# Optimization experiments

Hardware: AMD Instinct MI355X
Metric: run time of the kernel (lower is better)

The kernel has to match this reference:

```python
import jax, jax.numpy as jnp
import numpy as np
import math

B, S, HID, NH = 2, 2048, 1024, 16
HD = HID // NH  # head_dim = 64
TEMPERATURE = 1.0


def setup_inputs() -> dict:
    key = jax.random.key(0)
    ks = jax.random.split(key, 6)
    w = lambda k: (jax.random.normal(k, (HID, HID), dtype=jnp.float32) * 0.02)
    return {
        "hidden_states": jax.random.normal(ks[0], (B, S, HID), dtype=jnp.float32),
        "attention_mask": jnp.ones((B, S), dtype=jnp.float32),
        "Wq": w(ks[1]), "bq": jnp.zeros((HID,), jnp.float32),
        "Wk": w(ks[2]), "bk": jnp.zeros((HID,), jnp.float32),
        "Wv": w(ks[3]), "bv": jnp.zeros((HID,), jnp.float32),
        "Wo": w(ks[4]), "bo": jnp.zeros((HID,), jnp.float32),
    }


def reference(hidden_states, attention_mask, Wq, bq, Wk, bk, Wv, bv, Wo, bo):
    b, s, hid = hidden_states.shape
    heads = lambda x: x.reshape(b, s, NH, HD).transpose(0, 2, 1, 3)  # [b,h,s,d]

    q = heads(hidden_states @ Wq.T + bq)
    k = heads(hidden_states @ Wk.T + bk)
    v = heads(hidden_states @ Wv.T + bv)

    # padding mask applied multiplicatively to k and v
    m = attention_mask[:, None, :, None]  # [b,1,s,1]
    k = k * m
    v = v * m

    # auxiliary Hopfield state: k^T @ v per head -> [b,h,d,d]
    state = jnp.einsum("bhsd,bhse->bhde", k, v)

    # energy / scores
    energy = jnp.einsum("bhqd,bhkd->bhqk", q, k) / (TEMPERATURE * math.sqrt(HD))
    causal = jnp.triu(jnp.ones((s, s), dtype=bool), k=1)  # True above diagonal
    energy = jnp.where(causal[None, None], -jnp.inf, energy)
    energy = jnp.where(attention_mask[:, None, None, :] == 0, -jnp.inf, energy)

    attn = jax.nn.softmax(energy, axis=-1)
    out = jnp.einsum("bhqk,bhkd->bhqd", attn, v)
    out = out.transpose(0, 2, 1, 3).reshape(b, s, hid)
    out = out @ Wo.T + bo
    return out, state
```

## Files before the change

### kernel.cpp

```cpp
#include <hip/hip_runtime.h>
#include <hip/hip_bf16.h>

#define B_ 2
#define S_ 2048
#define HID_ 1024
#define NH_ 16
#define HD_ 64
#define MTOK (B_*S_)
#define LDQKV 3072

typedef __attribute__((ext_vector_type(8))) __bf16 bf16x8;
typedef __attribute__((ext_vector_type(4))) __bf16 bf16x4;
typedef __attribute__((ext_vector_type(4))) float f32x4;

__device__ __forceinline__ void gl16(__bf16* lds, const __bf16* g) {
  __builtin_amdgcn_global_load_lds(
      (const __attribute__((address_space(1))) void*)g,
      (__attribute__((address_space(3))) void*)lds, 16, 0, 0);
}

__global__ __launch_bounds__(256) void cast_all(
    const float* __restrict__ X,
    const float* __restrict__ Wq, const float* __restrict__ Wk,
    const float* __restrict__ Wv, const float* __restrict__ Wo,
    __bf16* __restrict__ Xb, __bf16* __restrict__ Wqkvb, __bf16* __restrict__ Wob)
{
  int i = blockIdx.x * 256 + threadIdx.x;
  const float* src; __bf16* dst; int j;
  if (i < (1 << 20))              { src = X;  dst = Xb;                 j = i; }
  else if (i < (1<<20)+(1<<18))   { src = Wq; dst = Wqkvb;              j = i - (1<<20); }
  else if (i < (1<<20)+(2<<18))   { src = Wk; dst = Wqkvb + (1<<20);    j = i - (1<<20) - (1<<18); }
  else if (i < (1<<20)+(3<<18))   { src = Wv; dst = Wqkvb + (2<<20);    j = i - (1<<20) - (2<<18); }
  else                            { src = Wo; dst = Wob;                j = i - (1<<20) - (3<<18); }
  float4 v = reinterpret_cast<const float4*>(src)[j];
  bf16x4 o;
  o[0] = (__bf16)v.x; o[1] = (__bf16)v.y; o[2] = (__bf16)v.z; o[3] = (__bf16)v.w;
  reinterpret_cast<bf16x4*>(dst)[j] = o;
}

__global__ __launch_bounds__(256) void gemm_qkv(
    const __bf16* __restrict__ A, const __bf16* __restrict__ W,
    const float* __restrict__ bq, const float* __restrict__ bk,
    const float* __restrict__ bv, const float* __restrict__ mask,
    __bf16* __restrict__ C)
{
  __shared__ __bf16 As[2][128 * 32];
  __shared__ __bf16 Bs[2][128 * 32];
  const int t = threadIdx.x;
  const int m0 = blockIdx.y * 128;
  const int n0 = blockIdx.x * 128;
  const int lane = t & 63;
  const int w = t >> 6;
  const int wr = (w >> 1) * 64;
  const int wc = (w & 1) * 64;
  const int fr = lane & 15;
  const int kg = lane >> 4;

  f32x4 acc[4][4];
  #pragma unroll
  for (int i = 0; i < 4; i++)
    #pragma unroll
    for (int j = 0; j < 4; j++) acc[i][j] = (f32x4)0.f;

  const int srow = w * 16 + (lane >> 2);
  const int scol = (lane & 3) * 8;
  const __bf16* ap0 = A + (size_t)(m0 + srow) * HID_ + scol;
  const __bf16* ap1 = A + (size_t)(m0 + 64 + srow) * HID_ + scol;
  const __bf16* wp0 = W + (size_t)(n0 + srow) * HID_ + scol;
  const __bf16* wp1 = W + (size_t)(n0 + 64 + srow) * HID_ + scol;

  #define GSTAGE(buf, koff) \
    gl16(&As[buf][w * 512], ap0 + (koff)); \
    gl16(&As[buf][2048 + w * 512], ap1 + (koff)); \
    gl16(&Bs[buf][w * 512], wp0 + (koff)); \
    gl16(&Bs[buf][2048 + w * 512], wp1 + (koff));

  GSTAGE(0, 0);
  for (int k0 = 0; k0 < HID_; k0 += 32) {
    const int cur = (k0 >> 5) & 1;
    if (k0 + 32 < HID_) {
      GSTAGE(cur ^ 1, k0 + 32);
      asm volatile("s_waitcnt vmcnt(4)" ::: "memory");
    } else {
      asm volatile("s_waitcnt vmcnt(0)" ::: "memory");
    }
    __builtin_amdgcn_sched_barrier(0);
    __builtin_amdgcn_s_barrier();
    bf16x8 af[4], bf[4];
    #pragma unroll
    for (int m = 0; m < 4; m++) af[m] = *(const bf16x8*)&As[cur][(wr + m*16 + fr) * 32 + kg*8];
    #pragma unroll
    for (int n = 0; n < 4; n++) bf[n] = *(const bf16x8*)&Bs[cur][(wc + n*16 + fr) * 32 + kg*8];
    #pragma unroll
    for (int m = 0; m < 4; m++)
      #pragma unroll
      for (int n = 0; n < 4; n++)
        acc[m][n] = __builtin_amdgcn_mfma_f32_16x16x32_bf16(af[m], bf[n], acc[m][n], 0, 0, 0);
    __builtin_amdgcn_s_barrier();
  }

  const int region = n0 >> 10;
  const float* bias = region == 0 ? bq : (region == 1 ? bk : bv);
  const int nloc = n0 & 1023;

  #pragma unroll
  for (int m = 0; m < 4; m++) {
    #pragma unroll
    for (int r = 0; r < 4; r++) {
      int row = m0 + wr + m*16 + kg*4 + r;
      float rs = region ? mask[row] : 1.f;
      #pragma unroll
      for (int n = 0; n < 4; n++) {
        int c = wc + n*16 + fr;
        float v = (acc[m][n][r] + bias[nloc + c]) * rs;
        C[(size_t)row * LDQKV + n0 + c] = (__bf16)v;
      }
    }
  }
}

__global__ __launch_bounds__(256) void gemm_o(
    const __bf16* __restrict__ A, const __bf16* __restrict__ W,
    const float* __restrict__ bias, float* __restrict__ C)
{
  __shared__ __bf16 As[2][128 * 32];
  __shared__ __bf16 Bs[2][128 * 32];
  const int t = threadIdx.x;
  const int m0 = blockIdx.y * 128;
  const int n0 = blockIdx.x * 128;
  const int lane = t & 63;
  const int w = t >> 6;
  const int wr = (w >> 1) * 64;
  const int wc = (w & 1) * 64;
  const int fr = lane & 15;
  const int kg = lane >> 4;

  f32x4 acc[4][4];
  #pragma unroll
  for (int i = 0; i < 4; i++)
    #pragma unroll
    for (int j = 0; j < 4; j++) acc[i][j] = (f32x4)0.f;

  const int srow = w * 16 + (lane >> 2);
  const int scol = (lane & 3) * 8;
  const __bf16* ap0 = A + (size_t)(m0 + srow) * HID_ + scol;
  const __bf16* ap1 = A + (size_t)(m0 + 64 + srow) * HID_ + scol;
  const __bf16* wp0 = W + (size_t)(n0 + srow) * HID_ + scol;
  const __bf16* wp1 = W + (size_t)(n0 + 64 + srow) * HID_ + scol;

  GSTAGE(0, 0);
  for (int k0 = 0; k0 < HID_; k0 += 32) {
    const int cur = (k0 >> 5) & 1;
    if (k0 + 32 < HID_) {
      GSTAGE(cur ^ 1, k0 + 32);
      asm volatile("s_waitcnt vmcnt(4)" ::: "memory");
    } else {
      asm volatile("s_waitcnt vmcnt(0)" ::: "memory");
    }
    __builtin_amdgcn_sched_barrier(0);
    __builtin_amdgcn_s_barrier();
    bf16x8 af[4], bf[4];
    #pragma unroll
    for (int m = 0; m < 4; m++) af[m] = *(const bf16x8*)&As[cur][(wr + m*16 + fr) * 32 + kg*8];
    #pragma unroll
    for (int n = 0; n < 4; n++) bf[n] = *(const bf16x8*)&Bs[cur][(wc + n*16 + fr) * 32 + kg*8];
    #pragma unroll
    for (int m = 0; m < 4; m++)
      #pragma unroll
      for (int n = 0; n < 4; n++)
        acc[m][n] = __builtin_amdgcn_mfma_f32_16x16x32_bf16(af[m], bf[n], acc[m][n], 0, 0, 0);
    __builtin_amdgcn_s_barrier();
  }

  #pragma unroll
  for (int m = 0; m < 4; m++) {
    #pragma unroll
    for (int r = 0; r < 4; r++) {
      int row = m0 + wr + m*16 + kg*4 + r;
      #pragma unroll
      for (int n = 0; n < 4; n++) {
        int col = n0 + wc + n*16 + fr;
        C[(size_t)row * HID_ + col] = acc[m][n][r] + bias[col];
      }
    }
  }
}

__global__ __launch_bounds__(256) void transpose_kv(
    const __bf16* __restrict__ Kin, const __bf16* __restrict__ Vin,
    __bf16* __restrict__ Kt, __bf16* __restrict__ Vt)
{
  __shared__ __bf16 tile[64][68];
  const int tok0 = blockIdx.x * 64;
  const int f0 = blockIdx.y * 64;
  const __bf16* in = blockIdx.z ? Vin : Kin;
  __bf16* out = blockIdx.z ? Vt : Kt;
  const int t = threadIdx.x;
  const int r = t >> 2;
  const int c0 = (t & 3) * 16;
  const __bf16* src = in + (size_t)(tok0 + r) * LDQKV + f0 + c0;
  *(bf16x8*)&tile[r][c0]     = *(const bf16x8*)src;
  *(bf16x8*)&tile[r][c0 + 8] = *(const bf16x8*)(src + 8);
  __syncthreads();
  bf16x8 o0, o1;
  #pragma unroll
  for (int j = 0; j < 8; j++) { o0[j] = tile[c0 + j][r]; o1[j] = tile[c0 + 8 + j][r]; }
  __bf16* dst = out + (size_t)(f0 + r) * MTOK + tok0 + c0;
  *(bf16x8*)dst = o0;
  *(bf16x8*)(dst + 8) = o1;
}

#define SCALE_LOG2E 0.18033688011112043f

__device__ __forceinline__ bf16x8 ld_swz(const __bf16* base, int row, int xb) {
  return *(const bf16x8*)((const char*)base + row * 128 + (xb ^ ((row & 7) << 4)));
}
__device__ __forceinline__ void st_swz16(__bf16* base, int row, int colbyte, __bf16 v) {
  *(__bf16*)((char*)base + row * 128 + (colbyte ^ ((row & 7) << 4))) = v;
}
__device__ __forceinline__ bf16x8 ld_swz256(const __bf16* base, int row, int xb) {
  return *(const bf16x8*)((const char*)base + row * 256 + (xb ^ ((row & 7) << 4)));
}

__device__ __forceinline__ void attn_tile(
    const __bf16* __restrict__ ks, const __bf16* __restrict__ vs,
    const bool (&okm)[4], __bf16* __restrict__ pw,
    const bf16x8 (&qa)[2], f32x4 (&acc)[4], f32x4& accl,
    const bf16x8 ones, int q0w, int kt, int fc, int kg)
{
  f32x4 s[4];
  #pragma unroll
  for (int n = 0; n < 4; n++) s[n] = (f32x4)0.f;
  #pragma unroll
  for (int kd = 0; kd < 2; kd++)
    #pragma unroll
    for (int n = 0; n < 4; n++) {
      bf16x8 kf = ld_swz(ks, n * 16 + fc, kd * 64 + kg * 16);
      s[n] = __builtin_amdgcn_mfma_f32_16x16x32_bf16(qa[kd], kf, s[n], 0, 0, 0);
    }

  const int g4 = kg * 4;
  const bool fullt = (kt * 64 + 63 <= q0w);
  if (fullt) {
    #pragma unroll
    for (int r = 0; r < 4; r++)
      #pragma unroll
      for (int n = 0; n < 4; n++) {
        float p = okm[n] ? __builtin_amdgcn_exp2f(s[n][r] * SCALE_LOG2E) : 0.f;
        st_swz16(pw, g4 + r, (n * 16 + fc) * 2, (__bf16)p);
      }
  } else {
    #pragma unroll
    for (int r = 0; r < 4; r++) {
      const int qg = q0w + g4 + r;
      #pragma unroll
      for (int n = 0; n < 4; n++) {
        bool ok = okm[n] && (kt * 64 + n * 16 + fc <= qg);
        float p = ok ? __builtin_amdgcn_exp2f(s[n][r] * SCALE_LOG2E) : 0.f;
        st_swz16(pw, g4 + r, (n * 16 + fc) * 2, (__bf16)p);
      }
    }
  }

  #pragma unroll
  for (int kc = 0; kc < 2; kc++) {
    bf16x8 pf = ld_swz(pw, fc, kc * 64 + kg * 16);
    accl = __builtin_amdgcn_mfma_f32_16x16x32_bf16(pf, ones, accl, 0, 0, 0);
    #pragma unroll
    for (int n = 0; n < 4; n++) {
      bf16x8 vf = ld_swz(vs, n * 16 + fc, kc * 64 + kg * 16);
      acc[n] = __builtin_amdgcn_mfma_f32_16x16x32_bf16(pf, vf, acc[n], 0, 0, 0);
    }
  }
}

__global__ __launch_bounds__(256) void flash_mfma(
    const __bf16* __restrict__ Q, const __bf16* __restrict__ K,
    const __bf16* __restrict__ Vt, const float* __restrict__ mask,
    __bf16* __restrict__ O)
{
  __shared__ __bf16 Ks[2][64 * 64];
  __shared__ __bf16 Vs[2][64 * 64];
  __shared__ __bf16 Ps[4][16 * 64];

  const int bh = blockIdx.x;
  const int qt = 31 - (int)blockIdx.y;
  const int b = bh >> 4, h = bh & 15;
  const int t = threadIdx.x;
  const int w = t >> 6;
  const int lane = t & 63;
  const int fc = lane & 15;
  const int kg = lane >> 4;
  const int g4 = kg * 4;

  const int q0w = qt * 64 + w * 16;
  const size_t tokbase = (size_t)b * S_;

  const int rr = lane >> 3;
  const int cswz = ((lane & 7) ^ rr) * 8;
  const int ktmax = qt;

  bf16x8 qa[2];
  {
    const __bf16* qp = Q + (tokbase + q0w + fc) * LDQKV + h * HD_;
    qa[0] = *(const bf16x8*)(qp + kg * 8);
    qa[1] = *(const bf16x8*)(qp + 32 + kg * 8);
  }

  const float* mp = mask + tokbase + fc;
  float mnxt[4];
  #pragma unroll
  for (int n = 0; n < 4; n++) mnxt[n] = mp[n * 16];

  const __bf16* kp0 = K + (tokbase + (size_t)(w * 16 + rr)) * LDQKV + h * HD_ + cswz;
  const __bf16* kp1 = kp0 + (size_t)8 * LDQKV;
  const __bf16* vp0 = Vt + (size_t)(h * HD_ + w * 16 + rr) * MTOK + tokbase + cswz;
  const __bf16* vp1 = vp0 + (size_t)8 * MTOK;

  gl16(&Ks[0][(w * 16) * 64],     kp0);
  gl16(&Ks[0][(w * 16 + 8) * 64], kp1);
  gl16(&Vs[0][(w * 16) * 64],     vp0);
  gl16(&Vs[0][(w * 16 + 8) * 64], vp1);
  kp0 += (size_t)64 * LDQKV; kp1 += (size_t)64 * LDQKV;
  vp0 += 64; vp1 += 64;

  bf16x8 ones;
  #pragma unroll
  for (int j = 0; j < 8; j++) ones[j] = (__bf16)1.f;

  f32x4 acc[4], accl;
  #pragma unroll
  for (int n = 0; n < 4; n++) acc[n] = (f32x4)0.f;
  accl = (f32x4)0.f;

  __bf16* pw = &Ps[w][0];

  for (int kt = 0; kt <= ktmax; ++kt) {
    const int cur = kt & 1;
    float mcur[4];
    #pragma unroll
    for (int n = 0; n < 4; n++) mcur[n] = mnxt[n];

    if (kt < ktmax) {
      #pragma unroll
      for (int n = 0; n < 4; n++) mnxt[n] = mp[(kt + 1) * 64 + n * 16];
      const int nxt = cur ^ 1;
      gl16(&Ks[nxt][(w * 16) * 64],     kp0);
      gl16(&Ks[nxt][(w * 16 + 8) * 64], kp1);
      gl16(&Vs[nxt][(w * 16) * 64],     vp0);
      gl16(&Vs[nxt][(w * 16 + 8) * 64], vp1);
      kp0 += (size_t)64 * LDQKV; kp1 += (size_t)64 * LDQKV;
      vp0 += 64; vp1 += 64;
      asm volatile("s_waitcnt vmcnt(8)" ::: "memory");
    } else {
      asm volatile("s_waitcnt vmcnt(0)" ::: "memory");
    }
    __builtin_amdgcn_sched_barrier(0);
    __builtin_amdgcn_s_barrier();

    bool okm[4];
    #pragma unroll
    for (int n = 0; n < 4; n++) okm[n] = (mcur[n] != 0.f);

    attn_tile(&Ks[cur][0], &Vs[cur][0], okm, pw, qa, acc, accl, ones, q0w, kt, fc, kg);

    __builtin_amdgcn_s_barrier();
  }

  #pragma unroll
  for (int r = 0; r < 4; r++) {
    float inv = accl[r] > 0.f ? 1.f / accl[r] : 0.f;
    __bf16* op = O + (tokbase + q0w + g4 + r) * HID_ + h * HD_;
    #pragma unroll
    for (int n = 0; n < 4; n++)
      op[n * 16 + fc] = (__bf16)(acc[n][r] * inv);
  }
}

__global__ __launch_bounds__(256) void state_mfma(
    const __bf16* __restrict__ Kt, const __bf16* __restrict__ Vt,
    float* __restrict__ part)
{
  __shared__ __bf16 Kl[64 * 128];
  __shared__ __bf16 Vl[64 * 128];
  const int bh = blockIdx.x, sc = blockIdx.y;
  const int b = bh >> 4, h = bh & 15;
  const int t = threadIdx.x;
  const int w = t >> 6;
  const int lane = t & 63;
  const int fc = lane & 15;
  const int kg = lane >> 4;
  const size_t colbase = (size_t)b * S_ + sc * 128;
  const int rloc = lane >> 4;
  const int cb = (lane & 15) * 16;

  #pragma unroll
  for (int c = 0; c < 4; c++) {
    int row = w * 16 + c * 4 + rloc;
    int scol = (cb ^ ((row & 7) << 4)) >> 1;
    gl16(&Kl[(w * 16 + c * 4) * 128], Kt + (size_t)(h * HD_ + row) * MTOK + colbase + scol);
    gl16(&Vl[(w * 16 + c * 4) * 128], Vt + (size_t)(h * HD_ + row) * MTOK + colbase + scol);
  }
  __syncthreads();

  f32x4 acc[4];
  #pragma unroll
  for (int n = 0; n < 4; n++) acc[n] = (f32x4)0.f;
  #pragma unroll
  for (int ks = 0; ks < 4; ks++) {
    bf16x8 af = ld_swz256(Kl, w * 16 + fc, ks * 64 + kg * 16);
    #pragma unroll
    for (int n = 0; n < 4; n++) {
      bf16x8 bfr = ld_swz256(Vl, n * 16 + fc, ks * 64 + kg * 16);
      acc[n] = __builtin_amdgcn_mfma_f32_16x16x32_bf16(af, bfr, acc[n], 0, 0, 0);
    }
  }

  float* dst = part + (((size_t)bh * 16 + sc) << 12);
  #pragma unroll
  for (int n = 0; n < 4; n++)
    #pragma unroll
    for (int r = 0; r < 4; r++)
      dst[(w * 16 + kg * 4 + r) * 64 + n * 16 + fc] = acc[n][r];
}

__global__ __launch_bounds__(256) void state_reduce(
    const float* __restrict__ part, float* __restrict__ out)
{
  int i = blockIdx.x * 256 + threadIdx.x;
  int bh = i >> 12, de = i & 4095;
  float s = 0.f;
  #pragma unroll
  for (int sc = 0; sc < 16; sc++) s += part[(((size_t)bh * 16 + sc) << 12) + de];
  out[i] = s;
}

extern "C" void kernel_launch(void* const* d_in, const int* in_sizes, int n_in,
                              void* d_out, int out_size, void* d_ws, size_t ws_size,
                              hipStream_t stream)
{
  const float* hs   = (const float*)d_in[0];
  const float* mask = (const float*)d_in[1];
  const float* Wq   = (const float*)d_in[2];
  const float* bq   = (const float*)d_in[3];
  const float* Wk   = (const float*)d_in[4];
  const float* bk   = (const float*)d_in[5];
  const float* Wv   = (const float*)d_in[6];
  const float* bv   = (const float*)d_in[7];
  const float* Wo   = (const float*)d_in[8];
  const float* bo   = (const float*)d_in[9];
  float* out = (float*)d_out;

  char* ws = (char*)d_ws;
  __bf16* Wqkvb = (__bf16*)(ws);
  __bf16* Wob   = (__bf16*)(ws + (6u  << 20));
  __bf16* Xb    = (__bf16*)(ws + (8u  << 20));
  __bf16* QKV   = (__bf16*)(ws + (16u << 20));
  __bf16* Ob    = (__bf16*)(ws + (40u << 20));
  __bf16* Ktg   = (__bf16*)(ws + (48u << 20));

  cast_all<<<8192, 256, 0, stream>>>(hs, Wq, Wk, Wv, Wo, Xb, Wqkvb, Wob);

  gemm_qkv<<<dim3(LDQKV / 128, MTOK / 128), 256, 0, stream>>>(
      Xb, Wqkvb, bq, bk, bv, mask, QKV);

  __bf16* Vtg = Xb;
  transpose_kv<<<dim3(MTOK / 64, HID_ / 64, 2), 256, 0, stream>>>(
      QKV + 1024, QKV + 2048, Ktg, Vtg);

  flash_mfma<<<dim3(B_ * NH_, 32), 256, 0, stream>>>(
      QKV, QKV + 1024, Vtg, mask, Ob);

  gemm_o<<<dim3(HID_ / 128, MTOK / 128), 256, 0, stream>>>(Ob, Wob, bo, out);

  float* part = (float*)Ob;
  state_mfma<<<dim3(B_ * NH_, 16), 256, 0, stream>>>(Ktg, Vtg, part);
  state_reduce<<<512, 256, 0, stream>>>(part, out + (size_t)MTOK * HID_);
}
```

Before: 136.0 us.

## Fuse K transpose into QKV GEMM and state reduction into output GEMM

The QKV GEMM epilogue now writes K transposed through a swizzled LDS tile, so the separate transpose only handles V. The state partial reduction is folded into extra blocks of the output projection GEMM. state_mfma processes two chunks per block, halving the partials to reduce. s_setprio is raised around the MFMA sections in the flash attention kernel. Together these cut kernel launches and intermediate traffic, at the cost of a longer epilogue on the K-region GEMM blocks and some load imbalance.

```diff
diff --git a/kernel.cpp b/kernel.cpp
--- a/kernel.cpp
+++ b/kernel.cpp
@@ -38,12 +38,166 @@
   reinterpret_cast<bf16x4*>(dst)[j] = o;
 }
 
+__device__ __forceinline__ void st_T(__bf16* T, int row, int col, __bf16 v) {
+  *(__bf16*)((char*)T + row * 256 + ((col * 2) ^ (((row >> 3) & 15) << 4))) = v;
+}
+__device__ __forceinline__ __bf16 ld_T(const __bf16* T, int row, int col) {
+  return *(const __bf16*)((const char*)T + row * 256 + ((col * 2) ^ (((row >> 3) & 15) << 4)));
+}
+
 __global__ __launch_bounds__(256) void gemm_qkv(
     const __bf16* __restrict__ A, const __bf16* __restrict__ W,
     const float* __restrict__ bq, const float* __restrict__ bk,
     const float* __restrict__ bv, const float* __restrict__ mask,
-    __bf16* __restrict__ C)
-{
+    __bf16* __restrict__ C, __bf16* __restrict__ Kt)
+{
+  __shared__ __bf16 SMEM[16384];
+  __bf16* As0 = SMEM;
+  __bf16* Bs0 = SMEM + 8192;
+  const int t = threadIdx.x;
+  const int m0 = blockIdx.y * 128;
+  const int n0 = blockIdx.x * 128;
+  const int lane = t & 63;
+  const int w = t >> 6;
+  const int wr = (w >> 1) * 64;
+  const int wc = (w & 1) * 64;
+  const int fr = lane & 15;
+  const int kg = lane >> 4;
+
+  f32x4 acc[4][4];
+  #pragma unroll
+  for (int i = 0; i < 4; i++)
+    #pragma unroll
+    for (int j = 0; j < 4; j++) acc[i][j] = (f32x4)0.f;
+
+  const int srow = w * 16 + (lane >> 2);
+  const int scol = (lane & 3) * 8;
+  const __bf16* ap0 = A + (size_t)(m0 + srow) * HID_ + scol;
+  const __bf16* ap1 = A + (size_t)(m0 + 64 + srow) * HID_ + scol;
+  const __bf16* wp0 = W + (size_t)(n0 + srow) * HID_ + scol;
+  const __bf16* wp1 = W + (size_t)(n0 + 64 + srow) * HID_ + scol;
+
+  #define GSTAGE(buf, koff) \
+    gl16(As0 + (buf)*4096 + w * 512, ap0 + (koff)); \
+    gl16(As0 + (buf)*4096 + 2048 + w * 512, ap1 + (koff)); \
+    gl16(Bs0 + (buf)*4096 + w * 512, wp0 + (koff)); \
+    gl16(Bs0 + (buf)*4096 + 2048 + w * 512, wp1 + (koff));
+
+  GSTAGE(0, 0);
+  for (int k0 = 0; k0 < HID_; k0 += 32) {
+    const int cur = (k0 >> 5) & 1;
+    if (k0 + 32 < HID_) {
+      GSTAGE(cur ^ 1, k0 + 32);
+      asm volatile("s_waitcnt vmcnt(4)" ::: "memory");
+    } else {
+      asm volatile("s_waitcnt vmcnt(0)" ::: "memory");
+    }
+    __builtin_amdgcn_sched_barrier(0);
+    __builtin_amdgcn_s_barrier();
+    bf16x8 af[4], bf[4];
+    #pragma unroll
+    for (int m = 0; m < 4; m++) af[m] = *(const bf16x8*)&As0[cur*4096 + (wr + m*16 + fr) * 32 + kg*8];
+    #pragma unroll
+    for (int n = 0; n < 4; n++) bf[n] = *(const bf16x8*)&Bs0[cur*4096 + (wc + n*16 + fr) * 32 + kg*8];
+    #pragma unroll
+    for (int m = 0; m < 4; m++)
+      #pragma unroll
+      for (int n = 0; n < 4; n++)
+        acc[m][n] = __builtin_amdgcn_mfma_f32_16x16x32_bf16(af[m], bf[n], acc[m][n], 0, 0, 0);
+    __builtin_amdgcn_s_barrier();
+  }
+
+  const int region = n0 >> 10;
+  const float* bias = region == 0 ? bq : (region == 1 ? bk : bv);
+  const int nloc = n0 & 1023;
+
+  #pragma unroll
+  for (int m = 0; m < 4; m++) {
+    #pragma unroll
+    for (int r = 0; r < 4; r++) {
+      int row = m0 + wr + m*16 + kg*4 + r;
+      float rs = region ? mask[row] : 1.f;
+      #pragma unroll
+      for (int n = 0; n < 4; n++) {
+        int c = wc + n*16 + fr;
+        C[(size_t)row * LDQKV + n0 + c] = (__bf16)((acc[m][n][r] + bias[nloc + c]) * rs);
+      }
+    }
+  }
+
+  if (region != 1) return;
+
+  __syncthreads();
+  __bf16* T = SMEM;
+  #pragma unroll
+  for (int m = 0; m < 4; m++) {
+    #pragma unroll
+    for (int r = 0; r < 4; r++) {
+      int rl = wr + m*16 + kg*4 + r;
+      float rs = mask[m0 + rl];
+      #pragma unroll
+      for (int n = 0; n < 4; n++) {
+        int c = wc + n*16 + fr;
+        st_T(T, rl, c, (__bf16)((acc[m][n][r] + bias[nloc + c]) * rs));
+      }
+    }
+  }
+  __syncthreads();
+
+  const int fo = t >> 4;
+  const int tcx = t & 15;
+  #pragma unroll
+  for (int g = 0; g < 8; g++) {
+    int f = g * 16 + fo;
+    bf16x8 ov;
+    #pragma unroll
+    for (int u = 0; u < 8; u++) ov[u] = ld_T(T, tcx * 8 + u, f);
+    *(bf16x8*)(Kt + (size_t)(nloc + f) * MTOK + m0 + tcx * 8) = ov;
+  }
+}
+
+__global__ __launch_bounds__(256) void transpose_v(
+    const __bf16* __restrict__ Vin, __bf16* __restrict__ Vt)
+{
+  __shared__ __bf16 tile[64][68];
+  const int tok0 = blockIdx.x * 64;
+  const int f0 = blockIdx.y * 64;
+  const int t = threadIdx.x;
+  const int r = t >> 2;
+  const int c0 = (t & 3) * 16;
+  const __bf16* src = Vin + (size_t)(tok0 + r) * LDQKV + f0 + c0;
+  *(bf16x8*)&tile[r][c0]     = *(const bf16x8*)src;
+  *(bf16x8*)&tile[r][c0 + 8] = *(const bf16x8*)(src + 8);
+  __syncthreads();
+  bf16x8 o0, o1;
+  #pragma unroll
+  for (int j = 0; j < 8; j++) { o0[j] = tile[c0 + j][r]; o1[j] = tile[c0 + 8 + j][r]; }
+  __bf16* dst = Vt + (size_t)(f0 + r) * MTOK + tok0 + c0;
+  *(bf16x8*)dst = o0;
+  *(bf16x8*)(dst + 8) = o1;
+}
+
+__global__ __launch_bounds__(256) void gemm_o(
+    const __bf16* __restrict__ A, const __bf16* __restrict__ W,
+    const float* __restrict__ bias, const float* __restrict__ part,
+    float* __restrict__ C)
+{
+  if (blockIdx.y >= 32) {
+    const int bl = blockIdx.x + (blockIdx.y - 32) * 8;
+    const int tid = bl * 256 + threadIdx.x;
+    float* outState = C + (size_t)MTOK * HID_;
+    #pragma unroll 4
+    for (int e = 0; e < 32; e++) {
+      int i = e * 4096 + tid;
+      int bh = i >> 12, de = i & 4095;
+      float s = 0.f;
+      #pragma unroll
+      for (int sc = 0; sc < 8; sc++) s += part[(size_t)((bh << 3) + sc) * 4096 + de];
+      outState[i] = s;
+    }
+    return;
+  }
+
   __shared__ __bf16 As[2][128 * 32];
   __shared__ __bf16 Bs[2][128 * 32];
   const int t = threadIdx.x;
@@ -69,90 +223,17 @@
   const __bf16* wp0 = W + (size_t)(n0 + srow) * HID_ + scol;
   const __bf16* wp1 = W + (size_t)(n0 + 64 + srow) * HID_ + scol;
 
-  #define GSTAGE(buf, koff) \
+  #define GSTAGE2(buf, koff) \
     gl16(&As[buf][w * 512], ap0 + (koff)); \
     gl16(&As[buf][2048 + w * 512], ap1 + (koff)); \
     gl16(&Bs[buf][w * 512], wp0 + (koff)); \
     gl16(&Bs[buf][2048 + w * 512], wp1 + (koff));
 
-  GSTAGE(0, 0);
+  GSTAGE2(0, 0);
   for (int k0 = 0; k0 < HID_; k0 += 32) {
     const int cur = (k0 >> 5) & 1;
     if (k0 + 32 < HID_) {
-      GSTAGE(cur ^ 1, k0 + 32);
-      asm volatile("s_waitcnt vmcnt(4)" ::: "memory");
-    } else {
-      asm volatile("s_waitcnt vmcnt(0)" ::: "memory");
-    }
-    __builtin_amdgcn_sched_barrier(0);
-    __builtin_amdgcn_s_barrier();
-    bf16x8 af[4], bf[4];
-    #pragma unroll
-    for (int m = 0; m < 4; m++) af[m] = *(const bf16x8*)&As[cur][(wr + m*16 + fr) * 32 + kg*8];
-    #pragma unroll
-    for (int n = 0; n < 4; n++) bf[n] = *(const bf16x8*)&Bs[cur][(wc + n*16 + fr) * 32 + kg*8];
-    #pragma unroll
-    for (int m = 0; m < 4; m++)
-      #pragma unroll
-      for (int n = 0; n < 4; n++)
-        acc[m][n] = __builtin_amdgcn_mfma_f32_16x16x32_bf16(af[m], bf[n], acc[m][n], 0, 0, 0);
-    __builtin_amdgcn_s_barrier();
-  }
-
-  const int region = n0 >> 10;
-  const float* bias = region == 0 ? bq : (region == 1 ? bk : bv);
-  const int nloc = n0 & 1023;
-
-  #pragma unroll
-  for (int m = 0; m < 4; m++) {
-    #pragma unroll
-    for (int r = 0; r < 4; r++) {
-      int row = m0 + wr + m*16 + kg*4 + r;
-      float rs = region ? mask[row] : 1.f;
-      #pragma unroll
-      for (int n = 0; n < 4; n++) {
-        int c = wc + n*16 + fr;
-        float v = (acc[m][n][r] + bias[nloc + c]) * rs;
-        C[(size_t)row * LDQKV + n0 + c] = (__bf16)v;
-      }
-    }
-  }
-}
-
-__global__ __launch_bounds__(256) void gemm_o(
-    const __bf16* __restrict__ A, const __bf16* __restrict__ W,
-    const float* __restrict__ bias, float* __restrict__ C)
-{
-  __shared__ __bf16 As[2][128 * 32];
-  __shared__ __bf16 Bs[2][128 * 32];
-  const int t = threadIdx.x;
-  const int m0 = blockIdx.y * 128;
-  const int n0 = blockIdx.x * 128;
-  const int lane = t & 63;
-  const int w = t >> 6;
-  const int wr = (w >> 1) * 64;
-  const int wc = (w & 1) * 64;
-  const int fr = lane & 15;
-  const int kg = lane >> 4;
-
-  f32x4 acc[4][4];
-  #pragma unroll
-  for (int i = 0; i < 4; i++)
-    #pragma unroll
-    for (int j = 0; j < 4; j++) acc[i][j] = (f32x4)0.f;
-
-  const int srow = w * 16 + (lane >> 2);
-  const int scol = (lane & 3) * 8;
-  const __bf16* ap0 = A + (size_t)(m0 + srow) * HID_ + scol;
-  const __bf16* ap1 = A + (size_t)(m0 + 64 + srow) * HID_ + scol;
-  const __bf16* wp0 = W + (size_t)(n0 + srow) * HID_ + scol;
-  const __bf16* wp1 = W + (size_t)(n0 + 64 + srow) * HID_ + scol;
-
-  GSTAGE(0, 0);
-  for (int k0 = 0; k0 < HID_; k0 += 32) {
-    const int cur = (k0 >> 5) & 1;
-    if (k0 + 32 < HID_) {
-      GSTAGE(cur ^ 1, k0 + 32);
+      GSTAGE2(cur ^ 1, k0 + 32);
       asm volatile("s_waitcnt vmcnt(4)" ::: "memory");
     } else {
       asm volatile("s_waitcnt vmcnt(0)" ::: "memory");
@@ -184,30 +265,6 @@
       }
     }
   }
-}
-
-__global__ __launch_bounds__(256) void transpose_kv(
-    const __bf16* __restrict__ Kin, const __bf16* __restrict__ Vin,
-    __bf16* __restrict__ Kt, __bf16* __restrict__ Vt)
-{
-  __shared__ __bf16 tile[64][68];
-  const int tok0 = blockIdx.x * 64;
-  const int f0 = blockIdx.y * 64;
-  const __bf16* in = blockIdx.z ? Vin : Kin;
-  __bf16* out = blockIdx.z ? Vt : Kt;
-  const int t = threadIdx.x;
-  const int r = t >> 2;
-  const int c0 = (t & 3) * 16;
-  const __bf16* src = in + (size_t)(tok0 + r) * LDQKV + f0 + c0;
-  *(bf16x8*)&tile[r][c0]     = *(const bf16x8*)src;
-  *(bf16x8*)&tile[r][c0 + 8] = *(const bf16x8*)(src + 8);
-  __syncthreads();
-  bf16x8 o0, o1;
-  #pragma unroll
-  for (int j = 0; j < 8; j++) { o0[j] = tile[c0 + j][r]; o1[j] = tile[c0 + 8 + j][r]; }
-  __bf16* dst = out + (size_t)(f0 + r) * MTOK + tok0 + c0;
-  *(bf16x8*)dst = o0;
-  *(bf16x8*)(dst + 8) = o1;
 }
 
 #define SCALE_LOG2E 0.18033688011112043f
@@ -231,6 +288,7 @@
   f32x4 s[4];
   #pragma unroll
   for (int n = 0; n < 4; n++) s[n] = (f32x4)0.f;
+  __builtin_amdgcn_s_setprio(1);
   #pragma unroll
   for (int kd = 0; kd < 2; kd++)
     #pragma unroll
@@ -238,6 +296,7 @@
       bf16x8 kf = ld_swz(ks, n * 16 + fc, kd * 64 + kg * 16);
       s[n] = __builtin_amdgcn_mfma_f32_16x16x32_bf16(qa[kd], kf, s[n], 0, 0, 0);
     }
+  __builtin_amdgcn_s_setprio(0);
 
   const int g4 = kg * 4;
   const bool fullt = (kt * 64 + 63 <= q0w);
@@ -262,6 +321,7 @@
     }
   }
 
+  __builtin_amdgcn_s_setprio(1);
   #pragma unroll
   for (int kc = 0; kc < 2; kc++) {
     bf16x8 pf = ld_swz(pw, fc, kc * 64 + kg * 16);
@@ -272,6 +332,7 @@
       acc[n] = __builtin_amdgcn_mfma_f32_16x16x32_bf16(pf, vf, acc[n], 0, 0, 0);
     }
   }
+  __builtin_amdgcn_s_setprio(0);
 }
 
 __global__ __launch_bounds__(256) void flash_mfma(
@@ -390,49 +451,42 @@
   const int lane = t & 63;
   const int fc = lane & 15;
   const int kg = lane >> 4;
-  const size_t colbase = (size_t)b * S_ + sc * 128;
   const int rloc = lane >> 4;
   const int cb = (lane & 15) * 16;
 
-  #pragma unroll
-  for (int c = 0; c < 4; c++) {
-    int row = w * 16 + c * 4 + rloc;
-    int scol = (cb ^ ((row & 7) << 4)) >> 1;
-    gl16(&Kl[(w * 16 + c * 4) * 128], Kt + (size_t)(h * HD_ + row) * MTOK + colbase + scol);
-    gl16(&Vl[(w * 16 + c * 4) * 128], Vt + (size_t)(h * HD_ + row) * MTOK + colbase + scol);
-  }
-  __syncthreads();
-
   f32x4 acc[4];
   #pragma unroll
   for (int n = 0; n < 4; n++) acc[n] = (f32x4)0.f;
-  #pragma unroll
-  for (int ks = 0; ks < 4; ks++) {
-    bf16x8 af = ld_swz256(Kl, w * 16 + fc, ks * 64 + kg * 16);
-    #pragma unroll
-    for (int n = 0; n < 4; n++) {
-      bf16x8 bfr = ld_swz256(Vl, n * 16 + fc, ks * 64 + kg * 16);
-      acc[n] = __builtin_amdgcn_mfma_f32_16x16x32_bf16(af, bfr, acc[n], 0, 0, 0);
-    }
-  }
-
-  float* dst = part + (((size_t)bh * 16 + sc) << 12);
+
+  for (int ch = 0; ch < 2; ch++) {
+    const size_t colbase = (size_t)b * S_ + sc * 256 + ch * 128;
+    __syncthreads();
+    #pragma unroll
+    for (int c = 0; c < 4; c++) {
+      int row = w * 16 + c * 4 + rloc;
+      int scol = (cb ^ ((row & 7) << 4)) >> 1;
+      gl16(&Kl[(w * 16 + c * 4) * 128], Kt + (size_t)(h * HD_ + row) * MTOK + colbase + scol);
+      gl16(&Vl[(w * 16 + c * 4) * 128], Vt + (size_t)(h * HD_ + row) * MTOK + colbase + scol);
+    }
+    __syncthreads();
+
+    #pragma unroll
+    for (int ks = 0; ks < 4; ks++) {
+      bf16x8 af = ld_swz256(Kl, w * 16 + fc, ks * 64 + kg * 16);
+      #pragma unroll
+      for (int n = 0; n < 4; n++) {
+        bf16x8 bfr = ld_swz256(Vl, n * 16 + fc, ks * 64 + kg * 16);
+        acc[n] = __builtin_amdgcn_mfma_f32_16x16x32_bf16(af, bfr, acc[n], 0, 0, 0);
+      }
+    }
+  }
+
+  float* dst = part + ((size_t)((bh << 3) + sc) << 12);
   #pragma unroll
   for (int n = 0; n < 4; n++)
     #pragma unroll
     for (int r = 0; r < 4; r++)
       dst[(w * 16 + kg * 4 + r) * 64 + n * 16 + fc] = acc[n][r];
-}
-
-__global__ __launch_bounds__(256) void state_reduce(
-    const float* __restrict__ part, float* __restrict__ out)
-{
-  int i = blockIdx.x * 256 + threadIdx.x;
-  int bh = i >> 12, de = i & 4095;
-  float s = 0.f;
-  #pragma unroll
-  for (int sc = 0; sc < 16; sc++) s += part[(((size_t)bh * 16 + sc) << 12) + de];
-  out[i] = s;
 }
 
 extern "C" void kernel_launch(void* const* d_in, const int* in_sizes, int n_in,
@@ -462,18 +516,16 @@
   cast_all<<<8192, 256, 0, stream>>>(hs, Wq, Wk, Wv, Wo, Xb, Wqkvb, Wob);
 
   gemm_qkv<<<dim3(LDQKV / 128, MTOK / 128), 256, 0, stream>>>(
-      Xb, Wqkvb, bq, bk, bv, mask, QKV);
+      Xb, Wqkvb, bq, bk, bv, mask, QKV, Ktg);
 
   __bf16* Vtg = Xb;
-  transpose_kv<<<dim3(MTOK / 64, HID_ / 64, 2), 256, 0, stream>>>(
-      QKV + 1024, QKV + 2048, Ktg, Vtg);
+  transpose_v<<<dim3(MTOK / 64, HID_ / 64), 256, 0, stream>>>(QKV + 2048, Vtg);
 
   flash_mfma<<<dim3(B_ * NH_, 32), 256, 0, stream>>>(
       QKV, QKV + 1024, Vtg, mask, Ob);
 
-  gemm_o<<<dim3(HID_ / 128, MTOK / 128), 256, 0, stream>>>(Ob, Wob, bo, out);
-
-  float* part = (float*)Ob;
-  state_mfma<<<dim3(B_ * NH_, 16), 256, 0, stream>>>(Ktg, Vtg, part);
-  state_reduce<<<512, 256, 0, stream>>>(part, out + (size_t)MTOK * HID_);
-}
+  float* part = (float*)Wqkvb;
+  state_mfma<<<dim3(B_ * NH_, 8), 256, 0, stream>>>(Ktg, Vtg, part);
+
+  gemm_o<<<dim3(HID_ / 128, 34), 256, 0, stream>>>(Ob, Wob, bo, part, out);
+}
```

New measurement: 139.8 us. +2.8%, slower.
